# Kernel tuning notes

Measured on AMD Instinct MI355X. Metric: run time of the kernel, lower is better.

Reference implementation:

```python
import jax, jax.numpy as jnp
import numpy as np

N = 100000   # nodes
E = 1600000  # edges (avg degree 16)
D = 128      # in = hid = out dim
EPS = 1e-5   # BatchNorm eps


def setup_inputs() -> dict:
    key = jax.random.key(0)
    ks = jax.random.split(key, 14)
    x = jax.random.normal(ks[0], (N, D), dtype=jnp.float32)
    row = jax.random.randint(ks[1], (E,), 0, N, dtype=jnp.int32)
    col = jax.random.randint(ks[2], (E,), 0, N, dtype=jnp.int32)
    edge_weight = jax.random.uniform(ks[3], (E,), dtype=jnp.float32)
    s = 1.0 / np.sqrt(D)
    W0 = jax.random.uniform(ks[4], (D, D), jnp.float32, -s, s)
    b0 = jax.random.uniform(ks[5], (D,), jnp.float32, -s, s)
    W1 = jax.random.uniform(ks[6], (D, D), jnp.float32, -s, s)
    b1 = jax.random.uniform(ks[7], (D,), jnp.float32, -s, s)
    W2 = jax.random.uniform(ks[8], (D, D), jnp.float32, -s, s)
    b2 = jax.random.uniform(ks[9], (D,), jnp.float32, -s, s)
    g0 = jnp.ones((D,), jnp.float32); be0 = jnp.zeros((D,), jnp.float32)
    g1 = jnp.ones((D,), jnp.float32); be1 = jnp.zeros((D,), jnp.float32)
    return {"x": x, "edge_weight": edge_weight,
            "W0": W0, "b0": b0, "g0": g0, "be0": be0,
            "W1": W1, "b1": b1, "g1": g1, "be1": be1,
            "W2": W2, "b2": b2, "row": row, "col": col}


def _spmm(edge_weight, row, col, h):
    # (A_norm @ h) with A in COO: out[r] = sum_e w_e * h[col_e] for row_e == r
    return jax.ops.segment_sum(edge_weight[:, None] * h[col], row, num_segments=N)


def _bn(h, gamma, beta):
    # BatchNorm1d, training-mode stats (biased variance), over the node axis
    m = h.mean(axis=0)
    v = h.var(axis=0)
    return gamma * (h - m) * jax.lax.rsqrt(v + EPS) + beta


def reference(x, edge_weight, W0, b0, g0, be0, W1, b1, g1, be1, W2, b2, row, col):
    # hidden block 1: SpMM(A, Linear(h)) -> BN -> ReLU (dropout p=0)
    h = jax.nn.relu(_bn(_spmm(edge_weight, row, col, x @ W0 + b0), g0, be0))
    # hidden block 2
    h = jax.nn.relu(_bn(_spmm(edge_weight, row, col, h @ W1 + b1), g1, be1))
    # final layer: SpMM(A, Linear(h)), no BN/activation
    return _spmm(edge_weight, row, col, h @ W2 + b2)
```

## Files before the change

kernel.cpp:

```cpp
#include <hip/hip_runtime.h>
#include <cstddef>

#define DD 128
#define EPS 1e-5f

typedef short short8 __attribute__((ext_vector_type(8)));
typedef float float4v __attribute__((ext_vector_type(4)));

__device__ __forceinline__ unsigned short f2bf(float f) {
    union { float f; unsigned int u; } x; x.f = f;
    unsigned int r = x.u + 0x7fffu + ((x.u >> 16) & 1u);
    return (unsigned short)(r >> 16);
}
__device__ __forceinline__ float bfhi2f(unsigned int hi_bits) {
    union { unsigned int u; float f; } x; x.u = hi_bits;
    return x.f;
}


__global__ void hist_kernel(const int* __restrict__ row, int* __restrict__ deg, int E) {
    int e = blockIdx.x * blockDim.x + threadIdx.x;
    if (e < E) atomicAdd(&deg[row[e]], 1);
}

__global__ void scanA_kernel(const int* __restrict__ deg, int* __restrict__ tmp,
                             int* __restrict__ bsum, int n) {
    __shared__ int s[1024];
    int tid = threadIdx.x;
    int gid = blockIdx.x * 1024 + tid;
    int v = (gid < n) ? deg[gid] : 0;
    s[tid] = v;
    __syncthreads();
    for (int off = 1; off < 1024; off <<= 1) {
        int t = s[tid];
        int u = (tid >= off) ? s[tid - off] : 0;
        __syncthreads();
        s[tid] = t + u;
        __syncthreads();
    }
    if (gid < n) tmp[gid] = s[tid];
    if (tid == 1023) bsum[blockIdx.x] = s[1023];
}

__global__ void scanB_kernel(const int* __restrict__ bsum, int* __restrict__ boff,
                             int* __restrict__ row_start, int nb, int n) {
    __shared__ int s[128];
    int tid = threadIdx.x;
    int v = (tid < nb) ? bsum[tid] : 0;
    s[tid] = v;
    __syncthreads();
    for (int off = 1; off < 128; off <<= 1) {
        int t = s[tid];
        int u = (tid >= off) ? s[tid - off] : 0;
        __syncthreads();
        s[tid] = t + u;
        __syncthreads();
    }
    if (tid < nb) boff[tid] = s[tid] - v;
    if (tid == nb - 1) row_start[n] = s[tid];
}

__global__ void scanC_kernel(const int* __restrict__ deg, const int* __restrict__ tmp,
                             const int* __restrict__ boff, int* __restrict__ row_start,
                             int* __restrict__ cursor, int n) {
    int gid = blockIdx.x * 1024 + threadIdx.x;
    if (gid < n) {
        int rs = tmp[gid] - deg[gid] + boff[blockIdx.x];
        row_start[gid] = rs;
        cursor[gid] = rs;
    }
}

#define SCHUNK 2048

__global__ __launch_bounds__(256) void scatter_bucketed_kernel(
    const int* __restrict__ row, const int* __restrict__ col,
    const float* __restrict__ ew, int* __restrict__ cursor,
    unsigned long long* __restrict__ ebuf, int E, unsigned int bmagic) {
    int chunk = blockIdx.x >> 3;
    unsigned int bucket = blockIdx.x & 7;
    int base = chunk * SCHUNK + threadIdx.x;
    #pragma unroll
    for (int i = 0; i < SCHUNK / 256; ++i) {
        int e = base + i * 256;
        if (e < E) {
            int r = row[e];
            if (__umulhi((unsigned int)r, bmagic) == bucket) {
                int p = atomicAdd(&cursor[r], 1);
                unsigned long long pk = (unsigned long long)(unsigned int)col[e]
                                      | ((unsigned long long)__float_as_uint(ew[e]) << 32);
                ebuf[p] = pk;
            }
        }
    }
}


__global__ void convw_kernel(const float* __restrict__ W0, const float* __restrict__ W1,
                             const float* __restrict__ W2, unsigned short* __restrict__ T0,
                             unsigned short* __restrict__ T1, unsigned short* __restrict__ T2) {
    const float* W = (blockIdx.y == 0) ? W0 : (blockIdx.y == 1) ? W1 : W2;
    unsigned short* T = (blockIdx.y == 0) ? T0 : (blockIdx.y == 1) ? T1 : T2;
    int gid = blockIdx.x * 256 + threadIdx.x;
    int k = gid >> 7, n = gid & 127;
    T[n * DD + k] = f2bf(W[k * DD + n]);
}


__global__ __launch_bounds__(256) void gemm_mfma_f32_kernel(
    const float* __restrict__ A, const unsigned short* __restrict__ Wt,
    const float* __restrict__ bias, unsigned short* __restrict__ H, int nrows)
{
    __shared__ unsigned short Asl[64][136];
    __shared__ unsigned short Wsl[128][136];

    const int tid  = threadIdx.x;
    const int row0 = blockIdx.x * 64;

    for (int i = tid; i < 2048; i += 256) {
        int r = i >> 4, off = (i & 15) * 8;
        *(uint4*)&Wsl[r][off] = *(const uint4*)(Wt + (size_t)r * DD + off);
    }
    for (int i = tid; i < 2048; i += 256) {
        int r = i >> 5, off4 = i & 31;
        int grow = row0 + r;
        float4 v = make_float4(0.f, 0.f, 0.f, 0.f);
        if (grow < nrows)
            v = *(const float4*)(A + (size_t)grow * DD + off4 * 4);
        ushort4 p;
        p.x = f2bf(v.x); p.y = f2bf(v.y); p.z = f2bf(v.z); p.w = f2bf(v.w);
        *(ushort4*)&Asl[r][off4 * 4] = p;
    }
    __syncthreads();

    const int w = tid >> 6, lane = tid & 63;
    const int m = lane & 15, q = lane >> 4;

    short8 afr[4];
    #pragma unroll
    for (int c = 0; c < 4; ++c)
        afr[c] = *(const short8*)&Asl[w * 16 + m][c * 32 + q * 8];

    float4v acc[8];
    #pragma unroll
    for (int t = 0; t < 8; ++t) acc[t] = (float4v){0.f, 0.f, 0.f, 0.f};

    #pragma unroll
    for (int t = 0; t < 8; ++t) {
        #pragma unroll
        for (int c = 0; c < 4; ++c) {
            short8 bfr = *(const short8*)&Wsl[t * 16 + m][c * 32 + q * 8];
            acc[t] = __builtin_amdgcn_mfma_f32_16x16x32_bf16(afr[c], bfr, acc[t], 0, 0, 0);
        }
    }

    #pragma unroll
    for (int t = 0; t < 8; ++t) {
        float bv = bias[t * 16 + m];
        #pragma unroll
        for (int i = 0; i < 4; ++i)
            Asl[w * 16 + q * 4 + i][t * 16 + m] = f2bf(acc[t][i] + bv);
    }
    __syncthreads();

    for (int i = tid; i < 1024; i += 256) {
        int r = i >> 4, off = (i & 15) * 8;
        if (row0 + r < nrows)
            *(uint4*)(H + (size_t)(row0 + r) * DD + off) = *(const uint4*)&Asl[r][off];
    }
}


__global__ __launch_bounds__(256) void gemm_mfma_bf16_kernel(
    const unsigned int* __restrict__ A, const unsigned short* __restrict__ Wt,
    const float* __restrict__ bias,
    const float* __restrict__ sums, const float* __restrict__ g,
    const float* __restrict__ be,
    unsigned short* __restrict__ H, int nrows)
{
    __shared__ unsigned short Asl[64][136];
    __shared__ unsigned short Wsl[128][136];
    __shared__ float scl_s[128], sft_s[128];

    const int tid  = threadIdx.x;
    const int row0 = blockIdx.x * 64;

    if (tid < 128) {
        float inv_n = 1.0f / (float)nrows;
        float mean = sums[tid] * inv_n;
        float var = sums[128 + tid] * inv_n - mean * mean;
        float rstd = rsqrtf(var + EPS);
        float sc = g[tid] * rstd;
        scl_s[tid] = sc;
        sft_s[tid] = be[tid] - mean * sc;
    }

    for (int i = tid; i < 2048; i += 256) {
        int r = i >> 4, off = (i & 15) * 8;
        *(uint4*)&Wsl[r][off] = *(const uint4*)(Wt + (size_t)r * DD + off);
    }
    __syncthreads();

    for (int i = tid; i < 1024; i += 256) {
        int r = i >> 4, ch = (i & 15) * 8;
        int grow = row0 + r;
        uint4 u = make_uint4(0, 0, 0, 0);
        if (grow < nrows)
            u = *(const uint4*)(A + (size_t)grow * 64 + (ch >> 1));
        unsigned int uu[4] = {u.x, u.y, u.z, u.w};
        unsigned int outp[4];
        #pragma unroll
        for (int j = 0; j < 4; ++j) {
            float vx = bfhi2f(uu[j] << 16);
            float vy = bfhi2f(uu[j] & 0xffff0000u);
            int k = ch + j * 2;
            vx = fmaxf(0.f, vx * scl_s[k] + sft_s[k]);
            vy = fmaxf(0.f, vy * scl_s[k + 1] + sft_s[k + 1]);
            outp[j] = (unsigned int)f2bf(vx) | ((unsigned int)f2bf(vy) << 16);
        }
        *(uint4*)&Asl[r][ch] = *(const uint4*)outp;
    }
    __syncthreads();

    const int w = tid >> 6, lane = tid & 63;
    const int m = lane & 15, q = lane >> 4;

    short8 afr[4];
    #pragma unroll
    for (int c = 0; c < 4; ++c)
        afr[c] = *(const short8*)&Asl[w * 16 + m][c * 32 + q * 8];

    float4v acc[8];
    #pragma unroll
    for (int t = 0; t < 8; ++t) acc[t] = (float4v){0.f, 0.f, 0.f, 0.f};

    #pragma unroll
    for (int t = 0; t < 8; ++t) {
        #pragma unroll
        for (int c = 0; c < 4; ++c) {
            short8 bfr = *(const short8*)&Wsl[t * 16 + m][c * 32 + q * 8];
            acc[t] = __builtin_amdgcn_mfma_f32_16x16x32_bf16(afr[c], bfr, acc[t], 0, 0, 0);
        }
    }

    #pragma unroll
    for (int t = 0; t < 8; ++t) {
        float bv = bias[t * 16 + m];
        #pragma unroll
        for (int i = 0; i < 4; ++i)
            Asl[w * 16 + q * 4 + i][t * 16 + m] = f2bf(acc[t][i] + bv);
    }
    __syncthreads();

    for (int i = tid; i < 1024; i += 256) {
        int r = i >> 4, off = (i & 15) * 8;
        if (row0 + r < nrows)
            *(uint4*)(H + (size_t)(row0 + r) * DD + off) = *(const uint4*)&Asl[r][off];
    }
}


__global__ __launch_bounds__(256, 8) void spmm_bf16_kernel(
    const unsigned short* __restrict__ H, const int* __restrict__ row_start,
    const unsigned long long* __restrict__ ebuf,
    float* __restrict__ Sf, unsigned int* __restrict__ Sb, int writeBF, int N, int K)
{
    const int lane = threadIdx.x & 63;
    const int g = lane >> 4;
    const int p = lane & 15;
    const int wave = (blockIdx.x << 2) | (threadIdx.x >> 6);
    int r0 = wave * K;
    if (r0 >= N) return;
    int r1 = min(N, r0 + K);

    const unsigned short* Hp = H + p * 8;
    const unsigned long long* Ep = ebuf + g;

    for (int r = r0; r < r1; ++r) {
        int e = row_start[r];
        const int e1 = row_start[r + 1];
        float acc[8];
        #pragma unroll
        for (int j = 0; j < 8; ++j) acc[j] = 0.f;

        for (; e + 15 < e1; e += 16) {
            unsigned long long pk[4];
            #pragma unroll
            for (int j = 0; j < 4; ++j)
                pk[j] = __builtin_nontemporal_load(Ep + e + j * 4);
            uint4 u[4];
            #pragma unroll
            for (int j = 0; j < 4; ++j)
                u[j] = *(const uint4*)(Hp + (size_t)(unsigned int)pk[j] * DD);
            #pragma unroll
            for (int j = 0; j < 4; ++j) {
                float wj = __uint_as_float((unsigned int)(pk[j] >> 32));
                unsigned int uu[4] = {u[j].x, u[j].y, u[j].z, u[j].w};
                #pragma unroll
                for (int q = 0; q < 4; ++q) {
                    acc[2 * q]     += wj * bfhi2f(uu[q] << 16);
                    acc[2 * q + 1] += wj * bfhi2f(uu[q] & 0xffff0000u);
                }
            }
        }
        for (; e + 7 < e1; e += 8) {
            unsigned long long pk[2];
            #pragma unroll
            for (int j = 0; j < 2; ++j)
                pk[j] = __builtin_nontemporal_load(Ep + e + j * 4);
            uint4 u[2];
            #pragma unroll
            for (int j = 0; j < 2; ++j)
                u[j] = *(const uint4*)(Hp + (size_t)(unsigned int)pk[j] * DD);
            #pragma unroll
            for (int j = 0; j < 2; ++j) {
                float wj = __uint_as_float((unsigned int)(pk[j] >> 32));
                unsigned int uu[4] = {u[j].x, u[j].y, u[j].z, u[j].w};
                #pragma unroll
                for (int q = 0; q < 4; ++q) {
                    acc[2 * q]     += wj * bfhi2f(uu[q] << 16);
                    acc[2 * q + 1] += wj * bfhi2f(uu[q] & 0xffff0000u);
                }
            }
        }
        if (e + 3 < e1) {
            unsigned long long pk = __builtin_nontemporal_load(Ep + e);
            uint4 u = *(const uint4*)(Hp + (size_t)(unsigned int)pk * DD);
            float wj = __uint_as_float((unsigned int)(pk >> 32));
            unsigned int uu[4] = {u.x, u.y, u.z, u.w};
            #pragma unroll
            for (int q = 0; q < 4; ++q) {
                acc[2 * q]     += wj * bfhi2f(uu[q] << 16);
                acc[2 * q + 1] += wj * bfhi2f(uu[q] & 0xffff0000u);
            }
            e += 4;
        }
        if (e < e1) {
            int idx = e + g;
            unsigned long long pk = (idx < e1) ? __builtin_nontemporal_load(&ebuf[idx]) : 0ull;
            uint4 u = *(const uint4*)(Hp + (size_t)(unsigned int)pk * DD);
            float wj = __uint_as_float((unsigned int)(pk >> 32));
            unsigned int uu[4] = {u.x, u.y, u.z, u.w};
            #pragma unroll
            for (int q = 0; q < 4; ++q) {
                acc[2 * q]     += wj * bfhi2f(uu[q] << 16);
                acc[2 * q + 1] += wj * bfhi2f(uu[q] & 0xffff0000u);
            }
        }

        #pragma unroll
        for (int j = 0; j < 8; ++j) {
            acc[j] += __shfl_xor(acc[j], 16);
            acc[j] += __shfl_xor(acc[j], 32);
        }

        if (g == 0) {
            if (writeBF) {
                unsigned int o[4];
                #pragma unroll
                for (int j = 0; j < 4; ++j)
                    o[j] = (unsigned int)f2bf(acc[2 * j])
                         | ((unsigned int)f2bf(acc[2 * j + 1]) << 16);
                *(uint4*)(Sb + (size_t)r * 64 + p * 4) = *(const uint4*)o;
            } else {
                float4 lo = make_float4(acc[0], acc[1], acc[2], acc[3]);
                float4 hi = make_float4(acc[4], acc[5], acc[6], acc[7]);
                *(float4*)(Sf + (size_t)r * DD + p * 8) = lo;
                *(float4*)(Sf + (size_t)r * DD + p * 8 + 4) = hi;
            }
        }
    }
}


__global__ void bn_stats_bf16_kernel(const unsigned int* __restrict__ Sb,
                                     float* __restrict__ sums, int n) {
    __shared__ float lsx[256], lsx2[256], lsy[256], lsy2[256];
    int tid = threadIdx.x;
    int c2 = tid & 63;
    float sx = 0.f, sx2 = 0.f, sy = 0.f, sy2 = 0.f;
    int total = n * 64;
    for (int i = blockIdx.x * 256 + tid; i < total; i += 256 * 256) {
        unsigned int u = Sb[i];
        float vx = bfhi2f(u << 16);
        float vy = bfhi2f(u & 0xffff0000u);
        sx += vx; sx2 += vx * vx;
        sy += vy; sy2 += vy * vy;
    }
    lsx[tid] = sx; lsx2[tid] = sx2; lsy[tid] = sy; lsy2[tid] = sy2;
    __syncthreads();
    if (tid < 64) {
        sx  = lsx[tid]  + lsx[tid + 64]  + lsx[tid + 128]  + lsx[tid + 192];
        sx2 = lsx2[tid] + lsx2[tid + 64] + lsx2[tid + 128] + lsx2[tid + 192];
        sy  = lsy[tid]  + lsy[tid + 64]  + lsy[tid + 128]  + lsy[tid + 192];
        sy2 = lsy2[tid] + lsy2[tid + 64] + lsy2[tid + 128] + lsy2[tid + 192];
        atomicAdd(&sums[2 * c2], sx);
        atomicAdd(&sums[2 * c2 + 1], sy);
        atomicAdd(&sums[128 + 2 * c2], sx2);
        atomicAdd(&sums[129 + 2 * c2], sy2);
    }
}


extern "C" void kernel_launch(void* const* d_in, const int* in_sizes, int n_in,
                              void* d_out, int out_size, void* d_ws, size_t ws_size,
                              hipStream_t stream) {
    const float* x   = (const float*)d_in[0];
    const float* ew  = (const float*)d_in[1];
    const float* W0  = (const float*)d_in[2];
    const float* b0  = (const float*)d_in[3];
    const float* g0  = (const float*)d_in[4];
    const float* be0 = (const float*)d_in[5];
    const float* W1  = (const float*)d_in[6];
    const float* b1  = (const float*)d_in[7];
    const float* g1  = (const float*)d_in[8];
    const float* be1 = (const float*)d_in[9];
    const float* W2  = (const float*)d_in[10];
    const float* b2  = (const float*)d_in[11];
    const int* row   = (const int*)d_in[12];
    const int* col   = (const int*)d_in[13];

    const int N = in_sizes[0] / DD;
    const int E = in_sizes[1];
    float* out = (float*)d_out;

    char* w = (char*)d_ws;
    unsigned short* H   = (unsigned short*)w; w += (size_t)N * DD * 2;
    unsigned int* Sb    = (unsigned int*)w;   w += (size_t)N * 64 * 4;
    unsigned long long* ebuf = (unsigned long long*)w; w += (size_t)E * 8;
    unsigned short* Wt0 = (unsigned short*)w; w += DD * DD * 2;
    unsigned short* Wt1 = (unsigned short*)w; w += DD * DD * 2;
    unsigned short* Wt2 = (unsigned short*)w; w += DD * DD * 2;
    float* sums         = (float*)w;          w += 256 * 4;
    int*   deg          = (int*)w;            w += (size_t)N * 4;
    int*   tmp          = (int*)w;            w += (size_t)N * 4;
    int*   cursor       = (int*)w;            w += (size_t)N * 4;
    int*   bsum         = (int*)w;            w += 128 * 4;
    int*   boff         = (int*)w;            w += 128 * 4;
    int*   row_start    = (int*)w;            w += (size_t)(N + 1) * 4;

    unsigned int bmagic = (unsigned int)(((unsigned long long)8 << 32) / (unsigned long long)N);

    hipMemsetAsync(deg, 0, (size_t)N * 4, stream);
    hist_kernel<<<(E + 255) / 256, 256, 0, stream>>>(row, deg, E);
    int NB = (N + 1023) / 1024;
    scanA_kernel<<<NB, 1024, 0, stream>>>(deg, tmp, bsum, N);
    scanB_kernel<<<1, 128, 0, stream>>>(bsum, boff, row_start, NB, N);
    scanC_kernel<<<NB, 1024, 0, stream>>>(deg, tmp, boff, row_start, cursor, N);
    int nchunks = (E + SCHUNK - 1) / SCHUNK;
    scatter_bucketed_kernel<<<nchunks * 8, 256, 0, stream>>>(row, col, ew, cursor, ebuf, E, bmagic);

    convw_kernel<<<dim3(64, 3), 256, 0, stream>>>(W0, W1, W2, Wt0, Wt1, Wt2);

    int gblocks = (N + 63) / 64;

    const int SPMM_BLOCKS = 2048;
    const int totalWaves = SPMM_BLOCKS * 4;
    const int K = (N + totalWaves - 1) / totalWaves;

    gemm_mfma_f32_kernel<<<gblocks, 256, 0, stream>>>(x, Wt0, b0, H, N);
    spmm_bf16_kernel<<<SPMM_BLOCKS, 256, 0, stream>>>(H, row_start, ebuf, nullptr, Sb, 1, N, K);
    hipMemsetAsync(sums, 0, 256 * 4, stream);
    bn_stats_bf16_kernel<<<256, 256, 0, stream>>>(Sb, sums, N);

    gemm_mfma_bf16_kernel<<<gblocks, 256, 0, stream>>>(Sb, Wt1, b1, sums, g0, be0, H, N);
    spmm_bf16_kernel<<<SPMM_BLOCKS, 256, 0, stream>>>(H, row_start, ebuf, nullptr, Sb, 1, N, K);
    hipMemsetAsync(sums, 0, 256 * 4, stream);
    bn_stats_bf16_kernel<<<256, 256, 0, stream>>>(Sb, sums, N);

    gemm_mfma_bf16_kernel<<<gblocks, 256, 0, stream>>>(Sb, Wt2, b2, sums, g1, be1, H, N);
    spmm_bf16_kernel<<<SPMM_BLOCKS, 256, 0, stream>>>(H, row_start, ebuf, out, nullptr, 0, N, K);
}
```

Before: 599.2 us.

## Replace bucketed atomic scatter with two-phase coarse-bucket then LDS local sort

```diff
diff --git a/kernel.cpp b/kernel.cpp
--- a/kernel.cpp
+++ b/kernel.cpp
@@ -71,26 +71,62 @@
     }
 }
 
-#define SCHUNK 2048
-
-__global__ __launch_bounds__(256) void scatter_bucketed_kernel(
+
+__global__ void bcur_init_kernel(const int* __restrict__ row_start,
+                                 int* __restrict__ bcur, int nb) {
+    int b = blockIdx.x * 256 + threadIdx.x;
+    if (b < nb) bcur[b] = row_start[b << 7];
+}
+
+__global__ __launch_bounds__(256) void scatter_phase1_kernel(
     const int* __restrict__ row, const int* __restrict__ col,
-    const float* __restrict__ ew, int* __restrict__ cursor,
-    unsigned long long* __restrict__ ebuf, int E, unsigned int bmagic) {
-    int chunk = blockIdx.x >> 3;
-    unsigned int bucket = blockIdx.x & 7;
-    int base = chunk * SCHUNK + threadIdx.x;
-    #pragma unroll
-    for (int i = 0; i < SCHUNK / 256; ++i) {
-        int e = base + i * 256;
-        if (e < E) {
-            int r = row[e];
-            if (__umulhi((unsigned int)r, bmagic) == bucket) {
-                int p = atomicAdd(&cursor[r], 1);
-                unsigned long long pk = (unsigned long long)(unsigned int)col[e]
-                                      | ((unsigned long long)__float_as_uint(ew[e]) << 32);
-                ebuf[p] = pk;
-            }
+    const float* __restrict__ ew, int* __restrict__ bcur,
+    unsigned long long* __restrict__ ebuf2, int E) {
+    int e = blockIdx.x * 256 + threadIdx.x;
+    if (e >= E) return;
+    int r = row[e];
+    int p = atomicAdd(&bcur[r >> 7], 1);
+    unsigned long long pk = (unsigned long long)((unsigned int)col[e]
+                          | ((unsigned int)(r & 127) << 25))
+                          | ((unsigned long long)__float_as_uint(ew[e]) << 32);
+    ebuf2[p] = pk;
+}
+
+#define P2CAP 3072
+
+__global__ __launch_bounds__(256) void scatter_phase2_kernel(
+    const unsigned long long* __restrict__ ebuf2, const int* __restrict__ row_start,
+    int* __restrict__ cursor, unsigned long long* __restrict__ ebuf, int N) {
+    __shared__ int cur[128];
+    __shared__ unsigned long long outb[P2CAP];
+    int b = blockIdx.x;
+    int r_lo = b << 7;
+    int r_hi = min(N, r_lo + 128);
+    int e_lo = row_start[r_lo];
+    int e_hi = row_start[r_hi];
+    int cnt = e_hi - e_lo;
+    int tid = threadIdx.x;
+    if (cnt <= P2CAP) {
+        if (tid < 128) {
+            int r = r_lo + tid;
+            cur[tid] = (r < N) ? (row_start[r] - e_lo) : 0;
+        }
+        __syncthreads();
+        for (int i = e_lo + tid; i < e_hi; i += 256) {
+            unsigned long long pk = ebuf2[i];
+            int rl = (int)((unsigned int)(pk >> 25) & 127u);
+            int pos = atomicAdd(&cur[rl], 1);
+            outb[pos] = pk & 0xFFFFFFFF0001FFFFull;
+        }
+        __syncthreads();
+        for (int i = tid; i < cnt; i += 256)
+            ebuf[e_lo + i] = outb[i];
+    } else {
+        for (int i = e_lo + tid; i < e_hi; i += 256) {
+            unsigned long long pk = ebuf2[i];
+            int rl = (int)((unsigned int)(pk >> 25) & 127u);
+            int pos = atomicAdd(&cursor[r_lo + rl], 1);
+            ebuf[pos] = pk & 0xFFFFFFFF0001FFFFull;
         }
     }
 }
@@ -439,7 +475,9 @@
     int*   boff         = (int*)w;            w += 128 * 4;
     int*   row_start    = (int*)w;            w += (size_t)(N + 1) * 4;
 
-    unsigned int bmagic = (unsigned int)(((unsigned long long)8 << 32) / (unsigned long long)N);
+    unsigned long long* ebuf2 = (unsigned long long*)Sb;
+    int* bcur = tmp;
+    int nbuck = (N + 127) >> 7;
 
     hipMemsetAsync(deg, 0, (size_t)N * 4, stream);
     hist_kernel<<<(E + 255) / 256, 256, 0, stream>>>(row, deg, E);
@@ -447,8 +485,9 @@
     scanA_kernel<<<NB, 1024, 0, stream>>>(deg, tmp, bsum, N);
     scanB_kernel<<<1, 128, 0, stream>>>(bsum, boff, row_start, NB, N);
     scanC_kernel<<<NB, 1024, 0, stream>>>(deg, tmp, boff, row_start, cursor, N);
-    int nchunks = (E + SCHUNK - 1) / SCHUNK;
-    scatter_bucketed_kernel<<<nchunks * 8, 256, 0, stream>>>(row, col, ew, cursor, ebuf, E, bmagic);
+    bcur_init_kernel<<<(nbuck + 255) / 256, 256, 0, stream>>>(row_start, bcur, nbuck);
+    scatter_phase1_kernel<<<(E + 255) / 256, 256, 0, stream>>>(row, col, ew, bcur, ebuf2, E);
+    scatter_phase2_kernel<<<nbuck, 256, 0, stream>>>(ebuf2, row_start, cursor, ebuf, N);
 
     convw_kernel<<<dim3(64, 3), 256, 0, stream>>>(W0, W1, W2, Wt0, Wt1, Wt2);
 
```

Result: slower. 908.4 us (+51.6%).
